# Kernel tuning notes

Hardware: AMD Instinct MI355X
Metric: run time of the kernel (lower is better)

Reference implementation:

```python
import jax, jax.numpy as jnp
import numpy as np

SAMPLES = 8    # batch of sets
N = 1024       # set size == rows of the permutation-closed index matrix
K = 16         # number of distinct weight-sharing groups
M = N // K     # columns per group per row (rectangular splits)
CI = 128       # channels_in
CO = 256       # channels_out


def setup_inputs() -> dict:
    key = jax.random.key(0)
    kx, kw = jax.random.split(key)
    x = jax.random.normal(kx, (SAMPLES, N, CI), dtype=jnp.float32)
    # weightParameter: [k, channels_out, channels_in]
    W = jax.random.normal(kw, (K, CO, CI), dtype=jnp.float32)
    # Rebuild the circulant group structure that __init__ derives from
    # running_weight_matrix: row j of `indices` is roll(base, j), so the
    # columns of group g in row j are (pos_g + j) mod N.
    base = np.repeat(np.arange(K), M)                      # indices row 0, [N]
    pos = np.stack([np.where(base == g)[0] for g in range(K)])  # [K, M]
    splits = (pos[:, None, :] + np.arange(N)[None, :, None]) % N  # [K, N, M]
    return {"x": x, "W": W, "splits": jnp.asarray(splits, jnp.int32)}


def reference(x, W, splits):
    # sum-pool branch: result = sum_g ( sum_m x[:, splits[g]] ) @ W[g].T
    def body(acc, group):
        w, sp = group                      # w: [CO, CI], sp: [N, M]
        pooled = x[:, sp].sum(axis=2)      # gather [S, N, M, CI] -> [S, N, CI]
        return acc + jnp.einsum('snc,oc->sno', pooled, w), None

    init = jnp.zeros((x.shape[0], splits.shape[1], W.shape[1]), dtype=x.dtype)
    out, _ = jax.lax.scan(body, init, (W, splits))
    return out                             # [S, N, CO]
```

## Files before the change

### kernel.cpp

```cpp
#include <hip/hip_runtime.h>
#include <hip/hip_bf16.h>

#define S_   8
#define N_   1024
#define KG_  16
#define MW_  64
#define CI_  128
#define CO_  256

typedef __attribute__((ext_vector_type(8))) short bf16x8;
typedef __attribute__((ext_vector_type(4))) float f32x4;

__global__ __launch_bounds__(256) void win_kernel(const float* __restrict__ x,
                                                  const float* __restrict__ W,
                                                  __hip_bfloat16* __restrict__ win,
                                                  __hip_bfloat16* __restrict__ Wb) {
    __shared__ float lds[96][CI_];
    const int b   = blockIdx.x;
    const int tid = threadIdx.x;

    {
        const int wi = (b * 256 + tid) * 8;
        const float4 v0 = *(const float4*)&W[wi];
        const float4 v1 = *(const float4*)&W[wi + 4];
        union { unsigned short u[8]; uint4 v; } o;
        __hip_bfloat16 h;
        h = __float2bfloat16(v0.x); o.u[0] = *(unsigned short*)&h;
        h = __float2bfloat16(v0.y); o.u[1] = *(unsigned short*)&h;
        h = __float2bfloat16(v0.z); o.u[2] = *(unsigned short*)&h;
        h = __float2bfloat16(v0.w); o.u[3] = *(unsigned short*)&h;
        h = __float2bfloat16(v1.x); o.u[4] = *(unsigned short*)&h;
        h = __float2bfloat16(v1.y); o.u[5] = *(unsigned short*)&h;
        h = __float2bfloat16(v1.z); o.u[6] = *(unsigned short*)&h;
        h = __float2bfloat16(v1.w); o.u[7] = *(unsigned short*)&h;
        *(uint4*)&Wb[wi] = o.v;
    }

    const int s   = b >> 5;
    const int t0  = (b & 31) << 5;
    const float* xs = x + (size_t)s * N_ * CI_;

    for (int e = tid * 4; e < 96 * CI_; e += 256 * 4) {
        const int r = e >> 7;
        const int c = e & (CI_ - 1);
        *(float4*)&lds[r][c] = *(const float4*)&xs[((t0 + r) & (N_ - 1)) * CI_ + c];
    }
    __syncthreads();

    const int c  = tid & (CI_ - 1);
    const int tb = (tid >> 7) << 4;
    float s0 = 0.f, s1 = 0.f, s2 = 0.f, s3 = 0.f;
    #pragma unroll
    for (int m = 0; m < MW_; m += 4) {
        s0 += lds[tb + m + 0][c];
        s1 += lds[tb + m + 1][c];
        s2 += lds[tb + m + 2][c];
        s3 += lds[tb + m + 3][c];
    }
    float w = (s0 + s1) + (s2 + s3);
    __hip_bfloat16* wo = win + (size_t)s * N_ * CI_;
    wo[(t0 + tb) * CI_ + c] = __float2bfloat16(w);
    #pragma unroll
    for (int t = 1; t < 16; ++t) {
        w += lds[tb + t - 1 + MW_][c] - lds[tb + t - 1][c];
        wo[(t0 + tb + t) * CI_ + c] = __float2bfloat16(w);
    }
}

#define BKE  64
#define AST  (128 * BKE)
#define BST  (64  * BKE)
#define KSTEPS 32

__global__ __launch_bounds__(256) void gemm_kernel(const __hip_bfloat16* __restrict__ winb,
                                                   const __hip_bfloat16* __restrict__ Wb,
                                                   float* __restrict__ out) {
    __shared__ __align__(16) unsigned short Alds[2 * AST];
    __shared__ __align__(16) unsigned short Blds[2 * BST];

    const int tid = threadIdx.x;
    const int l   = tid & 63;
    const int wv  = tid >> 6;
    const int s   = blockIdx.x >> 3;
    const int n0  = (blockIdx.x & 7) << 7;
    const int o0  = blockIdx.y << 6;

    const int wm = wv >> 1;
    const int wn = wv & 1;
    const int fr = l & 15;
    const int kq = l >> 4;
    const int rl = l >> 3;
    const int ps = l & 7;

    const unsigned short* winp = (const unsigned short*)winb + (size_t)s * N_ * CI_;
    const unsigned short* Wp   = (const unsigned short*)Wb;

    f32x4 acc[4][2];
    #pragma unroll
    for (int i = 0; i < 4; ++i)
        #pragma unroll
        for (int j = 0; j < 2; ++j)
            acc[i][j] = f32x4{0.f, 0.f, 0.f, 0.f};

    auto stage = [&](int t, int buf) {
        const int g  = t >> 1;
        const int ch = (t & 1) << 6;
        unsigned short* Ab = &Alds[buf * AST];
        unsigned short* Bb = &Blds[buf * BST];
        #pragma unroll
        for (int q = 0; q < 4; ++q) {
            const int rb  = (wv * 4 + q) * 8;
            const int row = rb + rl;
            const int ss  = ps ^ (row & 7);
            const unsigned short* src =
                winp + (((n0 + (g << 6) + row) & (N_ - 1)) * CI_) + ch + ss * 8;
            __builtin_amdgcn_global_load_lds((const __attribute__((address_space(1))) void*)src,
                                             (__attribute__((address_space(3))) void*)(Ab + rb * BKE),
                                             16, 0, 0);
        }
        #pragma unroll
        for (int q = 0; q < 2; ++q) {
            const int rb  = (wv * 2 + q) * 8;
            const int row = rb + rl;
            const int ss  = ps ^ (row & 7);
            const unsigned short* src =
                Wp + ((g * CO_ + o0 + row) * CI_) + ch + ss * 8;
            __builtin_amdgcn_global_load_lds((const __attribute__((address_space(1))) void*)src,
                                             (__attribute__((address_space(3))) void*)(Bb + rb * BKE),
                                             16, 0, 0);
        }
    };

    stage(0, 0);

    for (int t = 0; t < KSTEPS; ++t) {
        const int cur = t & 1;
        if (t < KSTEPS - 1) {
            stage(t + 1, cur ^ 1);
            asm volatile("s_waitcnt vmcnt(6)" ::: "memory");
        } else {
            asm volatile("s_waitcnt vmcnt(0)" ::: "memory");
        }
        __builtin_amdgcn_sched_barrier(0);
        __builtin_amdgcn_s_barrier();

        const unsigned short* Ab = &Alds[cur * AST];
        const unsigned short* Bb = &Blds[cur * BST];
        #pragma unroll
        for (int ks = 0; ks < 2; ++ks) {
            const int sl = ks * 4 + kq;
            bf16x8 af[4], bfg[2];
            #pragma unroll
            for (int i = 0; i < 4; ++i) {
                const int row = wm * 64 + i * 16 + fr;
                af[i] = *(const bf16x8*)&Ab[row * BKE + ((sl ^ (row & 7)) * 8)];
            }
            #pragma unroll
            for (int j = 0; j < 2; ++j) {
                const int col = wn * 32 + j * 16 + fr;
                bfg[j] = *(const bf16x8*)&Bb[col * BKE + ((sl ^ (col & 7)) * 8)];
            }
            #pragma unroll
            for (int i = 0; i < 4; ++i)
                #pragma unroll
                for (int j = 0; j < 2; ++j)
                    acc[i][j] = __builtin_amdgcn_mfma_f32_16x16x32_bf16(af[i], bfg[j], acc[i][j], 0, 0, 0);
        }
        __builtin_amdgcn_sched_barrier(0);
        __builtin_amdgcn_s_barrier();
    }

    float* op = out + ((size_t)(s * N_ + n0 + wm * 64) * CO_) + o0 + wn * 32;
    #pragma unroll
    for (int i = 0; i < 4; ++i)
        #pragma unroll
        for (int j = 0; j < 2; ++j)
            #pragma unroll
            for (int r = 0; r < 4; ++r)
                op[(i * 16 + kq * 4 + r) * CO_ + j * 16 + fr] = acc[i][j][r];
}

extern "C" void kernel_launch(void* const* d_in, const int* in_sizes, int n_in,
                              void* d_out, int out_size, void* d_ws, size_t ws_size,
                              hipStream_t stream) {
    const float* x = (const float*)d_in[0];
    const float* W = (const float*)d_in[1];

    __hip_bfloat16* winb = (__hip_bfloat16*)d_ws;
    __hip_bfloat16* Wbb  = (__hip_bfloat16*)((char*)d_ws +
                              (size_t)S_ * N_ * CI_ * sizeof(__hip_bfloat16));
    float* out = (float*)d_out;

    win_kernel<<<256, 256, 0, stream>>>(x, W, winb, Wbb);
    gemm_kernel<<<dim3(64, 4), 256, 0, stream>>>(winb, Wbb, out);
}
```

Before: 98.21 us.

## Split GEMM K-loop across two wave pipes with LDS reduction and doubled window buffer

```diff
diff --git a/kernel.cpp b/kernel.cpp
--- a/kernel.cpp
+++ b/kernel.cpp
@@ -58,42 +58,51 @@
         s3 += lds[tb + m + 3][c];
     }
     float w = (s0 + s1) + (s2 + s3);
-    __hip_bfloat16* wo = win + (size_t)s * N_ * CI_;
-    wo[(t0 + tb) * CI_ + c] = __float2bfloat16(w);
+    __hip_bfloat16* wo = win + (size_t)s * (2 * N_) * CI_;
+    {
+        const int row = t0 + tb;
+        const __hip_bfloat16 hv = __float2bfloat16(w);
+        wo[row * CI_ + c] = hv;
+        wo[(row + N_) * CI_ + c] = hv;
+    }
     #pragma unroll
     for (int t = 1; t < 16; ++t) {
         w += lds[tb + t - 1 + MW_][c] - lds[tb + t - 1][c];
-        wo[(t0 + tb + t) * CI_ + c] = __float2bfloat16(w);
+        const int row = t0 + tb + t;
+        const __hip_bfloat16 hv = __float2bfloat16(w);
+        wo[row * CI_ + c] = hv;
+        wo[(row + N_) * CI_ + c] = hv;
     }
 }
 
-#define BKE  64
-#define AST  (128 * BKE)
-#define BST  (64  * BKE)
-#define KSTEPS 32
-
-__global__ __launch_bounds__(256) void gemm_kernel(const __hip_bfloat16* __restrict__ winb,
-                                                   const __hip_bfloat16* __restrict__ Wb,
-                                                   float* __restrict__ out) {
-    __shared__ __align__(16) unsigned short Alds[2 * AST];
-    __shared__ __align__(16) unsigned short Blds[2 * BST];
-
-    const int tid = threadIdx.x;
-    const int l   = tid & 63;
-    const int wv  = tid >> 6;
-    const int s   = blockIdx.x >> 3;
-    const int n0  = (blockIdx.x & 7) << 7;
-    const int o0  = blockIdx.y << 6;
-
-    const int wm = wv >> 1;
-    const int wn = wv & 1;
+#define KSTEPS 16
+
+__global__ __launch_bounds__(256, 2) void gemm_kernel(const __hip_bfloat16* __restrict__ winb,
+                                                      const __hip_bfloat16* __restrict__ Wb,
+                                                      float* __restrict__ out) {
+    __shared__ __align__(16) unsigned short smem[32768];
+
+    const int tid  = threadIdx.x;
+    const int l    = tid & 63;
+    const int wv   = tid >> 6;
+    const int pw   = wv & 1;
+    const int pipe = wv >> 1;
+    const int s    = blockIdx.x & 7;
+    const int rem  = blockIdx.x >> 3;
+    const int n0   = (rem & 15) << 6;
+    const int o0   = (rem >> 4) << 6;
+
     const int fr = l & 15;
     const int kq = l >> 4;
     const int rl = l >> 3;
     const int ps = l & 7;
 
-    const unsigned short* winp = (const unsigned short*)winb + (size_t)s * N_ * CI_;
+    const unsigned short* winp = (const unsigned short*)winb
+                               + ((size_t)s * 2 * N_ + n0) * CI_;
     const unsigned short* Wp   = (const unsigned short*)Wb;
+
+#define AELEM(P, B) (smem + ((P) * 2 + (B)) * 4096)
+#define BELEM(P, B) (smem + 16384 + ((P) * 2 + (B)) * 4096)
 
     f32x4 acc[4][2];
     #pragma unroll
@@ -103,30 +112,26 @@
             acc[i][j] = f32x4{0.f, 0.f, 0.f, 0.f};
 
     auto stage = [&](int t, int buf) {
-        const int g  = t >> 1;
+        const int g  = pipe * 8 + (t >> 1);
         const int ch = (t & 1) << 6;
-        unsigned short* Ab = &Alds[buf * AST];
-        unsigned short* Bb = &Blds[buf * BST];
+        unsigned short* Ab = AELEM(pipe, buf);
+        unsigned short* Bb = BELEM(pipe, buf);
         #pragma unroll
         for (int q = 0; q < 4; ++q) {
-            const int rb  = (wv * 4 + q) * 8;
-            const int row = rb + rl;
+            const int row = (pw * 4 + q) * 8 + rl;
             const int ss  = ps ^ (row & 7);
-            const unsigned short* src =
-                winp + (((n0 + (g << 6) + row) & (N_ - 1)) * CI_) + ch + ss * 8;
+            const unsigned short* src = winp + (g * MW_ + row) * CI_ + ch + ss * 8;
             __builtin_amdgcn_global_load_lds((const __attribute__((address_space(1))) void*)src,
-                                             (__attribute__((address_space(3))) void*)(Ab + rb * BKE),
+                                             (__attribute__((address_space(3))) void*)(Ab + ((pw * 4 + q) * 8) * 64),
                                              16, 0, 0);
         }
         #pragma unroll
-        for (int q = 0; q < 2; ++q) {
-            const int rb  = (wv * 2 + q) * 8;
-            const int row = rb + rl;
+        for (int q = 0; q < 4; ++q) {
+            const int row = (pw * 4 + q) * 8 + rl;
             const int ss  = ps ^ (row & 7);
-            const unsigned short* src =
-                Wp + ((g * CO_ + o0 + row) * CI_) + ch + ss * 8;
+            const unsigned short* src = Wp + ((g * CO_ + o0 + row) * CI_) + ch + ss * 8;
             __builtin_amdgcn_global_load_lds((const __attribute__((address_space(1))) void*)src,
-                                             (__attribute__((address_space(3))) void*)(Bb + rb * BKE),
+                                             (__attribute__((address_space(3))) void*)(Bb + ((pw * 4 + q) * 8) * 64),
                                              16, 0, 0);
         }
     };
@@ -137,28 +142,28 @@
         const int cur = t & 1;
         if (t < KSTEPS - 1) {
             stage(t + 1, cur ^ 1);
-            asm volatile("s_waitcnt vmcnt(6)" ::: "memory");
+            asm volatile("s_waitcnt vmcnt(8)" ::: "memory");
         } else {
             asm volatile("s_waitcnt vmcnt(0)" ::: "memory");
         }
         __builtin_amdgcn_sched_barrier(0);
         __builtin_amdgcn_s_barrier();
 
-        const unsigned short* Ab = &Alds[cur * AST];
-        const unsigned short* Bb = &Blds[cur * BST];
+        const unsigned short* Ab = AELEM(pipe, cur);
+        const unsigned short* Bb = BELEM(pipe, cur);
         #pragma unroll
         for (int ks = 0; ks < 2; ++ks) {
             const int sl = ks * 4 + kq;
             bf16x8 af[4], bfg[2];
             #pragma unroll
             for (int i = 0; i < 4; ++i) {
-                const int row = wm * 64 + i * 16 + fr;
-                af[i] = *(const bf16x8*)&Ab[row * BKE + ((sl ^ (row & 7)) * 8)];
+                const int ar = i * 16 + fr;
+                af[i] = *(const bf16x8*)&Ab[ar * 64 + ((sl ^ (ar & 7)) * 8)];
             }
             #pragma unroll
             for (int j = 0; j < 2; ++j) {
-                const int col = wn * 32 + j * 16 + fr;
-                bfg[j] = *(const bf16x8*)&Bb[col * BKE + ((sl ^ (col & 7)) * 8)];
+                const int br = pw * 32 + j * 16 + fr;
+                bfg[j] = *(const bf16x8*)&Bb[br * 64 + ((sl ^ (br & 7)) * 8)];
             }
             #pragma unroll
             for (int i = 0; i < 4; ++i)
@@ -170,14 +175,27 @@
         __builtin_amdgcn_s_barrier();
     }
 
-    float* op = out + ((size_t)(s * N_ + n0 + wm * 64) * CO_) + o0 + wn * 32;
+    float* red = (float*)smem;
     #pragma unroll
     for (int i = 0; i < 4; ++i)
         #pragma unroll
         for (int j = 0; j < 2; ++j)
             #pragma unroll
             for (int r = 0; r < 4; ++r)
-                op[(i * 16 + kq * 4 + r) * CO_ + j * 16 + fr] = acc[i][j][r];
+                red[((pipe * 64) + (i * 16 + kq * 4 + r)) * 68 + pw * 32 + j * 16 + fr]
+                    = acc[i][j][r];
+
+    __syncthreads();
+
+    const int row = tid >> 2;
+    const int cb  = (tid & 3) << 4;
+    float* op = out + ((size_t)(s * N_ + n0 + row) * CO_) + o0 + cb;
+    #pragma unroll
+    for (int q = 0; q < 4; ++q) {
+        const f32x4 v0 = *(const f32x4*)&red[(row) * 68 + cb + q * 4];
+        const f32x4 v1 = *(const f32x4*)&red[(64 + row) * 68 + cb + q * 4];
+        *(f32x4*)&op[q * 4] = v0 + v1;
+    }
 }
 
 extern "C" void kernel_launch(void* const* d_in, const int* in_sizes, int n_in,
@@ -188,9 +206,9 @@
 
     __hip_bfloat16* winb = (__hip_bfloat16*)d_ws;
     __hip_bfloat16* Wbb  = (__hip_bfloat16*)((char*)d_ws +
-                              (size_t)S_ * N_ * CI_ * sizeof(__hip_bfloat16));
+                              (size_t)S_ * 2 * N_ * CI_ * sizeof(__hip_bfloat16));
     float* out = (float*)d_out;
 
     win_kernel<<<256, 256, 0, stream>>>(x, W, winb, Wbb);
-    gemm_kernel<<<dim3(64, 4), 256, 0, stream>>>(winb, Wbb, out);
+    gemm_kernel<<<512, 256, 0, stream>>>(winb, Wbb, out);
 }
```

New measurement: 82.06 us. -16.4%, faster.
